# Performance work log

Measured on AMD Instinct MI355X. Metric: run time of the kernel, lower is better.

## Reference

```python
import jax, jax.numpy as jnp
import numpy as np

N_NODES = 100000
N_EDGES = 1600000
HID = 128


def setup_inputs() -> dict:
    key = jax.random.key(0)
    k1, k2, k3, k4, k5 = jax.random.split(key, 5)
    node_embeddings = jax.random.normal(k1, (N_NODES, HID), dtype=jnp.float32)
    src_idx = jax.random.randint(k2, (N_EDGES,), 0, N_NODES, dtype=jnp.int64)
    tgt_idx = jax.random.randint(k3, (N_EDGES,), 0, N_NODES, dtype=jnp.int64)
    # Params of the selected edge-type predictor (Linear(2h,h) -> ReLU -> Linear(h,1))
    W1 = jax.random.normal(k4, (2 * HID, HID), dtype=jnp.float32) * (1.0 / np.sqrt(2 * HID))
    b1 = jnp.zeros((HID,), dtype=jnp.float32)
    W2 = jax.random.normal(k5, (HID, 1), dtype=jnp.float32) * (1.0 / np.sqrt(HID))
    b2 = jnp.zeros((1,), dtype=jnp.float32)
    return {
        "node_embeddings": node_embeddings,
        "src_idx": src_idx,
        "tgt_idx": tgt_idx,
        "edge_type_idx": 0,
        "W1": W1,
        "b1": b1,
        "W2": W2,
        "b2": b2,
    }


def reference(node_embeddings, src_idx, tgt_idx, edge_type_idx, W1, b1, W2, b2):
    # edge_type_idx selects a predictor; params passed in are that predictor's.
    src_emb = node_embeddings[src_idx]  # [E, H]
    tgt_emb = node_embeddings[tgt_idx]  # [E, H]
    # cat([src,tgt]) @ W1 == src @ W1[:H] + tgt @ W1[H:]  (avoids materializing pair_feat)
    h = jax.nn.relu(src_emb @ W1[:HID] + tgt_emb @ W1[HID:] + b1)  # [E, H]
    out = h @ W2 + b2  # [E, 1]
    return out[:, 0]  # squeeze(-1) -> [E]
```

## Files before the change

kernel.cpp:

```cpp
#include <hip/hip_runtime.h>
#include <hip/hip_bf16.h>

#define HID 128

typedef __attribute__((ext_vector_type(8))) short short8;
typedef __attribute__((ext_vector_type(4))) float f32x4;
typedef __attribute__((ext_vector_type(16))) float f32x16;
typedef __attribute__((ext_vector_type(4))) unsigned int u32x4;
typedef __attribute__((ext_vector_type(2))) _Float16 h2;

__device__ __forceinline__ short f2bf(float x) {
    __bf16 b = (__bf16)x;
    return __builtin_bit_cast(short, b);
}


__global__ void pack_w1_uv_kernel(const float* __restrict__ W1, short* __restrict__ bpk2,
                                  int* __restrict__ zero128) {
    if (zero128 && blockIdx.x == 0 && threadIdx.x < 128) zero128[threadIdx.x] = 0;
    int t = blockIdx.x * 256 + threadIdx.x;
    int l    = t & 63;
    int ks   = (t >> 6) & 7;
    int nt   = (t >> 9) & 3;
    int half = t >> 11;
    int k0  = half * 128 + ks * 16 + (l >> 5) * 8;
    int col = nt * 32 + (l & 31);
    short8 v;
#pragma unroll
    for (int j = 0; j < 8; ++j)
        v[j] = f2bf(W1[(k0 + j) * HID + col]);
    *reinterpret_cast<short8*>(&bpk2[t * 8]) = v;
}

__global__ __launch_bounds__(512, 4) void uv_kernel(
    const float* __restrict__ emb,
    const short* __restrict__ bpk2,
    unsigned short* __restrict__ U,
    unsigned short* __restrict__ V,
    int Nn)
{
    __shared__ short lds_b[32768];

    const int tid = threadIdx.x;
    const int l   = tid & 63;
    const int wid = tid >> 6;
    const int wg  = wid >> 1;
    const int wn  = wid & 1;
    const int lc  = l & 31;
    const int hi  = l >> 5;

    {
        const u32x4* g = (const u32x4*)bpk2;
        u32x4* d = (u32x4*)lds_b;
#pragma unroll
        for (int i = 0; i < 8; ++i) d[i * 512 + tid] = g[i * 512 + tid];
    }
    __syncthreads();

    const int base = blockIdx.x * 128 + wg * 32;
    int nr = base + lc;
    if (nr >= Nn) nr = Nn - 1;

    f32x16 accU[2], accV[2];
#pragma unroll
    for (int n = 0; n < 2; ++n) { accU[n] = (f32x16)(0.f); accV[n] = (f32x16)(0.f); }

#pragma unroll
    for (int ks = 0; ks < 8; ++ks) {
        const float* p = emb + (size_t)nr * HID + ks * 16 + hi * 8;
        f32x4 x0 = *reinterpret_cast<const f32x4*>(p);
        f32x4 x1 = *reinterpret_cast<const f32x4*>(p + 4);
        short8 afr;
#pragma unroll
        for (int j = 0; j < 4; ++j) { afr[j] = f2bf(x0[j]); afr[4 + j] = f2bf(x1[j]); }
#pragma unroll
        for (int n = 0; n < 2; ++n) {
            const int nt = wn * 2 + n;
            short8 bU = *reinterpret_cast<const short8*>(&lds_b[(((0 + nt) * 8 + ks) * 64 + l) * 8]);
            short8 bV = *reinterpret_cast<const short8*>(&lds_b[(((4 + nt) * 8 + ks) * 64 + l) * 8]);
            accU[n] = __builtin_amdgcn_mfma_f32_32x32x16_bf16(afr, bU, accU[n], 0, 0, 0);
            accV[n] = __builtin_amdgcn_mfma_f32_32x32x16_bf16(afr, bV, accV[n], 0, 0, 0);
        }
    }

#pragma unroll
    for (int n = 0; n < 2; ++n) {
        const int col = wn * 64 + n * 32 + lc;
#pragma unroll
        for (int r = 0; r < 16; ++r) {
            const int row = (r & 3) + 8 * (r >> 2) + 4 * hi;
            const int node = base + row;
            if (node < Nn) {
                _Float16 hu = (_Float16)accU[n][r];
                _Float16 hv = (_Float16)accV[n][r];
                U[(size_t)node * HID + col] = __builtin_bit_cast(unsigned short, hu);
                V[(size_t)node * HID + col] = __builtin_bit_cast(unsigned short, hv);
            }
        }
    }
}

__global__ __launch_bounds__(256) void hist64_kernel(
    const void* __restrict__ src_raw, const void* __restrict__ tgt_raw,
    int E, float bscale, int* __restrict__ gh)
{
    __shared__ int lh[64];
    const int tid = threadIdx.x;
    if (tid < 64) lh[tid] = 0;
    __syncthreads();

    int i64f = 1;
    {
        const int* s32 = (const int*)src_raw;
#pragma unroll
        for (int i = 1; i < 32; i += 2) i64f &= (s32[i] == 0);
    }
    const int stride = gridDim.x * 256;
    for (int e = blockIdx.x * 256 + tid; e < E; e += stride) {
        int t = i64f ? (int)((const long long*)tgt_raw)[e]
                     : ((const int*)tgt_raw)[e];
        int b = (int)((float)t * bscale);
        b = b < 0 ? 0 : (b > 63 ? 63 : b);
        atomicAdd(&lh[b], 1);
    }
    __syncthreads();
    if (tid < 64 && lh[tid]) atomicAdd(&gh[tid], lh[tid]);
}

__global__ __launch_bounds__(256) void scatter64_kernel(
    const void* __restrict__ src_raw, const void* __restrict__ tgt_raw,
    int E, float bscale,
    const int* __restrict__ gh, int* __restrict__ cursor,
    int2* __restrict__ st, int* __restrict__ ei)
{
    __shared__ int lh[64], lh2[64], lo[64], grb[64], go[64];
    __shared__ int2 sST[2048];
    __shared__ int sE[2048];
    __shared__ unsigned char bkk[2048];

    const int tid = threadIdx.x;
    int i64f = 1;
    {
        const int* s32 = (const int*)src_raw;
#pragma unroll
        for (int i = 1; i < 32; i += 2) i64f &= (s32[i] == 0);
    }
    if (tid < 64) { lh[tid] = 0; lh2[tid] = 0; }
    __syncthreads();

    const int base = blockIdx.x * 2048;
    int myS[8], myT[8], myB[8];
#pragma unroll
    for (int k = 0; k < 8; ++k) {
        const int e = base + k * 256 + tid;
        myB[k] = -1;
        if (e < E) {
            int s, t;
            if (i64f) {
                s = (int)((const long long*)src_raw)[e];
                t = (int)((const long long*)tgt_raw)[e];
            } else {
                s = ((const int*)src_raw)[e];
                t = ((const int*)tgt_raw)[e];
            }
            int b = (int)((float)t * bscale);
            b = b < 0 ? 0 : (b > 63 ? 63 : b);
            myS[k] = s; myT[k] = t; myB[k] = b;
            atomicAdd(&lh[b], 1);
        }
    }
    __syncthreads();
    if (tid < 64) {
        int vl = lh[tid], vg = gh[tid];
        int il = vl, ig = vg;
#pragma unroll
        for (int off = 1; off < 64; off <<= 1) {
            int xl = __shfl_up(il, off, 64);
            int xg = __shfl_up(ig, off, 64);
            if (tid >= off) { il += xl; ig += xg; }
        }
        lo[tid] = il - vl;
        go[tid] = ig - vg;
        grb[tid] = (vl > 0) ? atomicAdd(&cursor[tid], vl) : 0;
    }
    __syncthreads();
#pragma unroll
    for (int k = 0; k < 8; ++k) {
        if (myB[k] >= 0) {
            const int b = myB[k];
            const int pl = lo[b] + atomicAdd(&lh2[b], 1);
            sST[pl] = make_int2(myS[k], myT[k]);
            sE[pl] = base + k * 256 + tid;
            bkk[pl] = (unsigned char)b;
        }
    }
    __syncthreads();
    const int total = lo[63] + lh[63];
    for (int i = tid; i < total; i += 256) {
        const int b = bkk[i];
        const int dst = go[b] + grb[b] + (i - lo[b]);
        st[dst] = sST[i];
        ei[dst] = sE[i];
    }
}

__global__ __launch_bounds__(256) void edge_pass_part_kernel(
    const unsigned short* __restrict__ U,
    const unsigned short* __restrict__ V,
    const int2* __restrict__ st,
    const int* __restrict__ ei,
    const int* __restrict__ gh,
    const float* __restrict__ b1,
    const float* __restrict__ W2,
    const float* __restrict__ b2,
    float* __restrict__ out,
    int per_x)
{
    __shared__ int sh_off8[9];

    const int tid = threadIdx.x;
    if (tid < 64) {
        int v = gh[tid];
        int inc = v;
#pragma unroll
        for (int off = 1; off < 64; off <<= 1) {
            int x = __shfl_up(inc, off, 64);
            if (tid >= off) inc += x;
        }
        if ((tid & 7) == 0) sh_off8[tid >> 3] = inc - v;
        if (tid == 63) sh_off8[8] = inc;
    }
    __syncthreads();

    const int l   = tid & 63;
    const int wid = tid >> 6;
    const int le  = l >> 4;
    const int lc  = l & 15;
    const int p   = blockIdx.x & 7;
    const int r   = blockIdx.x >> 3;

    const int pbeg = sh_off8[p];
    const int pend = sh_off8[p + 1];

    h2 b1p[4], w2p[4];
    {
        f32x4 a = *reinterpret_cast<const f32x4*>(b1 + lc * 8);
        f32x4 b = *reinterpret_cast<const f32x4*>(b1 + lc * 8 + 4);
        f32x4 c = *reinterpret_cast<const f32x4*>(W2 + lc * 8);
        f32x4 d = *reinterpret_cast<const f32x4*>(W2 + lc * 8 + 4);
#pragma unroll
        for (int j = 0; j < 2; ++j) {
            b1p[0][j] = (_Float16)a[j];     b1p[1][j] = (_Float16)a[2 + j];
            b1p[2][j] = (_Float16)b[j];     b1p[3][j] = (_Float16)b[2 + j];
            w2p[0][j] = (_Float16)c[j];     w2p[1][j] = (_Float16)c[2 + j];
            w2p[2][j] = (_Float16)d[j];     w2p[3][j] = (_Float16)d[2 + j];
        }
    }
    const float b2s = b2[0];
    const h2 zero2 = (h2)((_Float16)0.f);

    for (int base = pbeg + r * 64; base < pend; base += per_x * 64) {
        short8 ub[4], vb[4];
        int oid[4];
        bool live[4];
#pragma unroll
        for (int g = 0; g < 4; ++g) {
            int pos = base + wid * 16 + g * 4 + le;
            live[g] = (pos < pend);
            if (!live[g]) pos = base;
            const int2 pr = st[pos];
            oid[g] = ei[pos];
            ub[g] = *reinterpret_cast<const short8*>(U + (unsigned)pr.x * HID + lc * 8);
            vb[g] = *reinterpret_cast<const short8*>(V + (unsigned)pr.y * HID + lc * 8);
        }

#pragma unroll
        for (int g = 0; g < 4; ++g) {
            const unsigned int* uw = (const unsigned int*)&ub[g];
            const unsigned int* vw = (const unsigned int*)&vb[g];
            h2 s2 = zero2;
#pragma unroll
            for (int j = 0; j < 4; ++j) {
                h2 hu = __builtin_bit_cast(h2, uw[j]);
                h2 hv = __builtin_bit_cast(h2, vw[j]);
                h2 h  = hu + hv + b1p[j];
                h = __builtin_elementwise_max(h, zero2);
                s2 = s2 + h * w2p[j];
            }
            float s = (float)s2[0] + (float)s2[1];
#pragma unroll
            for (int w = 1; w < 16; w <<= 1)
                s += __shfl_xor(s, w, 16);
            if (lc == 0 && live[g])
                out[oid[g]] = s + b2s;
        }
    }
}

__global__ __launch_bounds__(256) void edge_pass_kernel(
    const unsigned short* __restrict__ U,
    const unsigned short* __restrict__ V,
    const void* __restrict__ src_raw,
    const void* __restrict__ tgt_raw,
    const float* __restrict__ b1,
    const float* __restrict__ W2,
    const float* __restrict__ b2,
    float* __restrict__ out,
    int E)
{
    const int tid = threadIdx.x;
    const int l   = tid & 63;
    const int wid = tid >> 6;
    const int le  = l >> 4;
    const int lc  = l & 15;

    int oddw = 0;
    {
        const int* s32 = (const int*)src_raw;
        if (l < 32) oddw = s32[2 * l + 1];
    }
    const bool i64f = (__ballot(oddw != 0) == 0ULL);

    h2 b1p[4], w2p[4];
    {
        f32x4 a = *reinterpret_cast<const f32x4*>(b1 + lc * 8);
        f32x4 b = *reinterpret_cast<const f32x4*>(b1 + lc * 8 + 4);
        f32x4 c = *reinterpret_cast<const f32x4*>(W2 + lc * 8);
        f32x4 d = *reinterpret_cast<const f32x4*>(W2 + lc * 8 + 4);
#pragma unroll
        for (int j = 0; j < 2; ++j) {
            b1p[0][j] = (_Float16)a[j];     b1p[1][j] = (_Float16)a[2 + j];
            b1p[2][j] = (_Float16)b[j];     b1p[3][j] = (_Float16)b[2 + j];
            w2p[0][j] = (_Float16)c[j];     w2p[1][j] = (_Float16)c[2 + j];
            w2p[2][j] = (_Float16)d[j];     w2p[3][j] = (_Float16)d[2 + j];
        }
    }
    const float b2s = b2[0];
    const h2 zero2 = (h2)((_Float16)0.f);

    const long long ebase = ((long long)blockIdx.x * 4 + wid) * 16;

    short8 ub[4], vb[4];
#pragma unroll
    for (int g = 0; g < 4; ++g) {
        long long e = ebase + g * 4 + le;
        if (e >= E) e = E - 1;
        long long si, ti;
        if (i64f) {
            si = ((const long long*)src_raw)[e];
            ti = ((const long long*)tgt_raw)[e];
        } else {
            si = ((const int*)src_raw)[e];
            ti = ((const int*)tgt_raw)[e];
        }
        ub[g] = *reinterpret_cast<const short8*>(U + (unsigned)si * HID + lc * 8);
        vb[g] = *reinterpret_cast<const short8*>(V + (unsigned)ti * HID + lc * 8);
    }

#pragma unroll
    for (int g = 0; g < 4; ++g) {
        const unsigned int* uw = (const unsigned int*)&ub[g];
        const unsigned int* vw = (const unsigned int*)&vb[g];
        h2 s2 = zero2;
#pragma unroll
        for (int j = 0; j < 4; ++j) {
            h2 hu = __builtin_bit_cast(h2, uw[j]);
            h2 hv = __builtin_bit_cast(h2, vw[j]);
            h2 h  = hu + hv + b1p[j];
            h = __builtin_elementwise_max(h, zero2);
            s2 = s2 + h * w2p[j];
        }
        float s = (float)s2[0] + (float)s2[1];
#pragma unroll
        for (int w = 1; w < 16; w <<= 1)
            s += __shfl_xor(s, w, 16);
        const long long e = ebase + g * 4 + le;
        if (lc == 0 && e < E)
            out[e] = s + b2s;
    }
}


__global__ void pack_w1_kernel(const float* __restrict__ W1, short* __restrict__ bpk) {
    int t = blockIdx.x * 256 + threadIdx.x;
    int f = (t >> 6) & 7;
    int l = t & 63;
    int n = t >> 9;
    int c = l & 15, kb = l >> 4;
    int k0 = f * 32 + kb * 8;
    short8 v;
#pragma unroll
    for (int j = 0; j < 8; ++j)
        v[j] = f2bf(W1[(k0 + j) * HID + n * 16 + c]);
    *reinterpret_cast<short8*>(&bpk[t * 8]) = v;
}

__global__ __launch_bounds__(256) void conv_emb_kernel(
    const float* __restrict__ emb, short* __restrict__ bemb, int n8) {
    int i = blockIdx.x * 256 + threadIdx.x;
    if (i >= n8) return;
    f32x4 x0 = *reinterpret_cast<const f32x4*>(emb + (size_t)i * 8);
    f32x4 x1 = *reinterpret_cast<const f32x4*>(emb + (size_t)i * 8 + 4);
    short8 v;
#pragma unroll
    for (int j = 0; j < 4; ++j) {
        v[j]     = f2bf(x0[j]);
        v[4 + j] = f2bf(x1[j]);
    }
    *reinterpret_cast<short8*>(&bemb[(size_t)i * 8]) = v;
}

template <int MODE>
__global__ __launch_bounds__(512, 4) void edge_head_kernel(
    const float* __restrict__ emb,
    const short* __restrict__ bemb,
    const void* __restrict__ src_raw,
    const void* __restrict__ tgt_raw,
    const float* __restrict__ W1,
    const float* __restrict__ b1,
    const float* __restrict__ W2,
    const float* __restrict__ b2,
    const short* __restrict__ bpk,
    float* __restrict__ out,
    int E)
{
    __shared__ short lds_b[32768];

    const int tid = threadIdx.x;

    int i64f = 1;
    {
        const int* s32 = (const int*)src_raw;
#pragma unroll
        for (int i = 1; i < 32; i += 2) i64f &= (s32[i] == 0);
    }

    if (MODE != 2) {
        const u32x4* g = (const u32x4*)bpk;
        u32x4* d = (u32x4*)lds_b;
#pragma unroll
        for (int i = 0; i < 8; ++i) d[i * 512 + tid] = g[i * 512 + tid];
    } else {
        for (int i = 0; i < 64; ++i) {
            int idx = i * 512 + tid;
            int col = idx & 127;
            int k   = idx >> 7;
            int n = col >> 4, cc = col & 15;
            int f = k >> 5, kb = (k >> 3) & 3, j = k & 7;
            int l2 = kb * 16 + cc;
            lds_b[(((n * 8 + f) * 64 + l2) << 3) + j] = f2bf(W1[idx]);
        }
    }
    __syncthreads();

    const int l = tid & 63;
    const int wid = tid >> 6;
    const int c = l & 15;
    const int g = l >> 4;
    const long long e0 = (long long)blockIdx.x * 256 + wid * 32;

    unsigned so[2], to[2];
#pragma unroll
    for (int m = 0; m < 2; ++m) {
        long long e = e0 + m * 16 + c;
        if (e >= E) e = E - 1;
        long long si, ti;
        if (i64f) {
            si = ((const long long*)src_raw)[e];
            ti = ((const long long*)tgt_raw)[e];
        } else {
            si = ((const int*)src_raw)[e];
            ti = ((const int*)tgt_raw)[e];
        }
        so[m] = (unsigned)si * HID;
        to[m] = (unsigned)ti * HID;
    }

    f32x4 acc[2][8];
#pragma unroll
    for (int m = 0; m < 2; ++m)
#pragma unroll
        for (int n = 0; n < 8; ++n)
            acc[m][n] = (f32x4){0.f, 0.f, 0.f, 0.f};

    const int koff = g * 8;
#pragma unroll
    for (int f = 0; f < 8; ++f) {
        short8 afr[2];
        const int k0 = (f & 3) * 32 + koff;
#pragma unroll
        for (int m = 0; m < 2; ++m) {
            const unsigned off = (f < 4 ? so[m] : to[m]) + k0;
            if (MODE == 0) {
                afr[m] = *reinterpret_cast<const short8*>(bemb + off);
            } else {
                f32x4 x0 = *reinterpret_cast<const f32x4*>(emb + off);
                f32x4 x1 = *reinterpret_cast<const f32x4*>(emb + off + 4);
                short8 t;
#pragma unroll
                for (int j = 0; j < 4; ++j) {
                    t[j]     = f2bf(x0[j]);
                    t[4 + j] = f2bf(x1[j]);
                }
                afr[m] = t;
            }
        }
#pragma unroll
        for (int n = 0; n < 8; ++n) {
            short8 bfr = *reinterpret_cast<const short8*>(&lds_b[((n * 8 + f) * 64 + l) * 8]);
#pragma unroll
            for (int m = 0; m < 2; ++m)
                acc[m][n] = __builtin_amdgcn_mfma_f32_16x16x32_bf16(afr[m], bfr, acc[m][n], 0, 0, 0);
        }
    }

    float b1v[8], w2v[8];
#pragma unroll
    for (int n = 0; n < 8; ++n) {
        b1v[n] = b1[n * 16 + c];
        w2v[n] = W2[n * 16 + c];
    }
    const float b2s = b2[0];

#pragma unroll
    for (int m = 0; m < 2; ++m) {
        float s[4] = {0.f, 0.f, 0.f, 0.f};
#pragma unroll
        for (int n = 0; n < 8; ++n) {
#pragma unroll
            for (int r = 0; r < 4; ++r)
                s[r] += fmaxf(acc[m][n][r] + b1v[n], 0.f) * w2v[n];
        }
#pragma unroll
        for (int w = 1; w < 16; w <<= 1) {
#pragma unroll
            for (int r = 0; r < 4; ++r)
                s[r] += __shfl_xor(s[r], w, 16);
        }
        if (c == 0) {
            const long long eb = e0 + m * 16 + g * 4;
#pragma unroll
            for (int r = 0; r < 4; ++r)
                if (eb + r < E) out[eb + r] = s[r] + b2s;
        }
    }
}

extern "C" void kernel_launch(void* const* d_in, const int* in_sizes, int n_in,
                              void* d_out, int out_size, void* d_ws, size_t ws_size,
                              hipStream_t stream) {
    const float* emb = (const float*)d_in[0];
    const void*  src = d_in[1];
    const void*  tgt = d_in[2];
    const float* W1 = (const float*)d_in[4];
    const float* b1 = (const float*)d_in[5];
    const float* W2 = (const float*)d_in[6];
    const float* b2 = (const float*)d_in[7];
    float* out = (float*)d_out;

    const int E  = in_sizes[1];
    const int Nn = in_sizes[0] / HID;

    const size_t uv_bytes = (size_t)Nn * HID * sizeof(short);
    const size_t off_gh   = 65536;
    const size_t off_U    = 65536 + 4096;
    const size_t off_V    = off_U + uv_bytes;
    const size_t off_st   = off_V + uv_bytes;
    const size_t off_ei   = off_st + (size_t)E * 8;
    const size_t need_part = off_ei + (size_t)E * 4;
    const size_t need_uv   = 65536 + 2 * uv_bytes;
    const size_t need_old  = 65536 + (size_t)in_sizes[0] * sizeof(short);

    if (ws_size >= need_part && E >= 4096) {
        short*          bpk2   = (short*)d_ws;
        int*            gh     = (int*)((char*)d_ws + off_gh);
        int*            cursor = gh + 64;
        unsigned short* U      = (unsigned short*)((char*)d_ws + off_U);
        unsigned short* Vv     = (unsigned short*)((char*)d_ws + off_V);
        int2*           st     = (int2*)((char*)d_ws + off_st);
        int*            ei     = (int*)((char*)d_ws + off_ei);

        const float bscale = 63.9999f / (float)Nn;

        pack_w1_uv_kernel<<<16, 256, 0, stream>>>(W1, bpk2, gh);
        hist64_kernel<<<256, 256, 0, stream>>>(src, tgt, E, bscale, gh);
        uv_kernel<<<(Nn + 127) / 128, 512, 0, stream>>>(emb, bpk2, U, Vv, Nn);
        scatter64_kernel<<<(E + 2047) / 2048, 256, 0, stream>>>(
            src, tgt, E, bscale, gh, cursor, st, ei);
        const int per_x = (E / 8 + 4096) / 64 + 2;
        edge_pass_part_kernel<<<per_x * 8, 256, 0, stream>>>(
            U, Vv, st, ei, gh, b1, W2, b2, out, per_x);
        return;
    }

    if (ws_size >= need_uv) {
        short*          bpk2 = (short*)d_ws;
        unsigned short* U    = (unsigned short*)((char*)d_ws + 65536);
        unsigned short* Vv   = (unsigned short*)((char*)d_ws + 65536 + uv_bytes);

        pack_w1_uv_kernel<<<16, 256, 0, stream>>>(W1, bpk2, nullptr);
        uv_kernel<<<(Nn + 127) / 128, 512, 0, stream>>>(emb, bpk2, U, Vv, Nn);
        edge_pass_kernel<<<(E + 63) / 64, 256, 0, stream>>>(U, Vv, src, tgt, b1, W2, b2, out, E);
        return;
    }

    short* bpk  = (short*)d_ws;
    short* bemb = (short*)((char*)d_ws + 65536);

    int mode;
    if (ws_size >= need_old)        mode = 0;
    else if (ws_size >= 65536)      mode = 1;
    else                            mode = 2;

    if (mode != 2)
        pack_w1_kernel<<<16, 256, 0, stream>>>(W1, bpk);
    if (mode == 0) {
        const int n8 = in_sizes[0] / 8;
        conv_emb_kernel<<<(n8 + 255) / 256, 256, 0, stream>>>(emb, bemb, n8);
    }

    const int grid = (E + 255) / 256;
    if (mode == 0)
        edge_head_kernel<0><<<grid, 512, 0, stream>>>(emb, bemb, src, tgt, W1, b1, W2, b2, bpk, out, E);
    else if (mode == 1)
        edge_head_kernel<1><<<grid, 512, 0, stream>>>(emb, bemb, src, tgt, W1, b1, W2, b2, bpk, out, E);
    else
        edge_head_kernel<2><<<grid, 512, 0, stream>>>(emb, bemb, src, tgt, W1, b1, W2, b2, bpk, out, E);
}
```

Before: 147.5 us.

## Pack edge records into 64-bit words and fuse W1 packing with histogram

Each sorted edge record now holds the edge id, source and target node in one 64-bit word, so one array replaces the separate int2 pair and edge-id arrays. This cuts scatter writes and edge-pass index reads from 12 to 8 bytes per edge and shrinks the scatter kernel's shared memory. The W1 packing kernel is merged into the histogram kernel, and zeroing of the histogram moves to a memset, removing one launch. The packed path only works while node count fits in 17 bits and edge count in 21 bits, so it is guarded by a check.

```diff
diff --git a/kernel.cpp b/kernel.cpp
--- a/kernel.cpp
+++ b/kernel.cpp
@@ -15,21 +15,48 @@
 }
 
 
-__global__ void pack_w1_uv_kernel(const float* __restrict__ W1, short* __restrict__ bpk2,
-                                  int* __restrict__ zero128) {
-    if (zero128 && blockIdx.x == 0 && threadIdx.x < 128) zero128[threadIdx.x] = 0;
-    int t = blockIdx.x * 256 + threadIdx.x;
-    int l    = t & 63;
-    int ks   = (t >> 6) & 7;
-    int nt   = (t >> 9) & 3;
-    int half = t >> 11;
-    int k0  = half * 128 + ks * 16 + (l >> 5) * 8;
-    int col = nt * 32 + (l & 31);
-    short8 v;
-#pragma unroll
-    for (int j = 0; j < 8; ++j)
-        v[j] = f2bf(W1[(k0 + j) * HID + col]);
-    *reinterpret_cast<short8*>(&bpk2[t * 8]) = v;
+__global__ __launch_bounds__(256) void hist_pack_kernel(
+    const float* __restrict__ W1, short* __restrict__ bpk2,
+    const void* __restrict__ src_raw, const void* __restrict__ tgt_raw,
+    int E, float bscale, int* __restrict__ gh)
+{
+    const int tid = threadIdx.x;
+
+    if (blockIdx.x < 16) {
+        int t = blockIdx.x * 256 + tid;
+        int l    = t & 63;
+        int ks   = (t >> 6) & 7;
+        int nt   = (t >> 9) & 3;
+        int half = t >> 11;
+        int k0  = half * 128 + ks * 16 + (l >> 5) * 8;
+        int col = nt * 32 + (l & 31);
+        short8 v;
+#pragma unroll
+        for (int j = 0; j < 8; ++j)
+            v[j] = f2bf(W1[(k0 + j) * HID + col]);
+        *reinterpret_cast<short8*>(&bpk2[t * 8]) = v;
+    }
+
+    __shared__ int lh[64];
+    if (tid < 64) lh[tid] = 0;
+    __syncthreads();
+
+    int i64f = 1;
+    {
+        const int* s32 = (const int*)src_raw;
+#pragma unroll
+        for (int i = 1; i < 32; i += 2) i64f &= (s32[i] == 0);
+    }
+    const int stride = gridDim.x * 256;
+    for (int e = blockIdx.x * 256 + tid; e < E; e += stride) {
+        int t = i64f ? (int)((const long long*)tgt_raw)[e]
+                     : ((const int*)tgt_raw)[e];
+        int b = (int)((float)t * bscale);
+        b = b < 0 ? 0 : (b > 63 ? 63 : b);
+        atomicAdd(&lh[b], 1);
+    }
+    __syncthreads();
+    if (tid < 64 && lh[tid]) atomicAdd(&gh[tid], lh[tid]);
 }
 
 __global__ __launch_bounds__(512, 4) void uv_kernel(
@@ -100,43 +127,14 @@
     }
 }
 
-__global__ __launch_bounds__(256) void hist64_kernel(
-    const void* __restrict__ src_raw, const void* __restrict__ tgt_raw,
-    int E, float bscale, int* __restrict__ gh)
-{
-    __shared__ int lh[64];
-    const int tid = threadIdx.x;
-    if (tid < 64) lh[tid] = 0;
-    __syncthreads();
-
-    int i64f = 1;
-    {
-        const int* s32 = (const int*)src_raw;
-#pragma unroll
-        for (int i = 1; i < 32; i += 2) i64f &= (s32[i] == 0);
-    }
-    const int stride = gridDim.x * 256;
-    for (int e = blockIdx.x * 256 + tid; e < E; e += stride) {
-        int t = i64f ? (int)((const long long*)tgt_raw)[e]
-                     : ((const int*)tgt_raw)[e];
-        int b = (int)((float)t * bscale);
-        b = b < 0 ? 0 : (b > 63 ? 63 : b);
-        atomicAdd(&lh[b], 1);
-    }
-    __syncthreads();
-    if (tid < 64 && lh[tid]) atomicAdd(&gh[tid], lh[tid]);
-}
-
 __global__ __launch_bounds__(256) void scatter64_kernel(
     const void* __restrict__ src_raw, const void* __restrict__ tgt_raw,
     int E, float bscale,
     const int* __restrict__ gh, int* __restrict__ cursor,
-    int2* __restrict__ st, int* __restrict__ ei)
+    unsigned long long* __restrict__ rec)
 {
     __shared__ int lh[64], lh2[64], lo[64], grb[64], go[64];
-    __shared__ int2 sST[2048];
-    __shared__ int sE[2048];
-    __shared__ unsigned char bkk[2048];
+    __shared__ unsigned long long sR[2048];
 
     const int tid = threadIdx.x;
     int i64f = 1;
@@ -189,26 +187,26 @@
         if (myB[k] >= 0) {
             const int b = myB[k];
             const int pl = lo[b] + atomicAdd(&lh2[b], 1);
-            sST[pl] = make_int2(myS[k], myT[k]);
-            sE[pl] = base + k * 256 + tid;
-            bkk[pl] = (unsigned char)b;
+            sR[pl] = (unsigned long long)(unsigned)(base + k * 256 + tid)
+                   | ((unsigned long long)(unsigned)myS[k] << 21)
+                   | ((unsigned long long)(unsigned)myT[k] << 38);
         }
     }
     __syncthreads();
     const int total = lo[63] + lh[63];
     for (int i = tid; i < total; i += 256) {
-        const int b = bkk[i];
-        const int dst = go[b] + grb[b] + (i - lo[b]);
-        st[dst] = sST[i];
-        ei[dst] = sE[i];
+        const unsigned long long r = sR[i];
+        const int t = (int)(r >> 38);
+        int b = (int)((float)t * bscale);
+        b = b < 0 ? 0 : (b > 63 ? 63 : b);
+        rec[go[b] + grb[b] + (i - lo[b])] = r;
     }
 }
 
 __global__ __launch_bounds__(256) void edge_pass_part_kernel(
     const unsigned short* __restrict__ U,
     const unsigned short* __restrict__ V,
-    const int2* __restrict__ st,
-    const int* __restrict__ ei,
+    const unsigned long long* __restrict__ rec,
     const int* __restrict__ gh,
     const float* __restrict__ b1,
     const float* __restrict__ W2,
@@ -268,10 +266,12 @@
             int pos = base + wid * 16 + g * 4 + le;
             live[g] = (pos < pend);
             if (!live[g]) pos = base;
-            const int2 pr = st[pos];
-            oid[g] = ei[pos];
-            ub[g] = *reinterpret_cast<const short8*>(U + (unsigned)pr.x * HID + lc * 8);
-            vb[g] = *reinterpret_cast<const short8*>(V + (unsigned)pr.y * HID + lc * 8);
+            const unsigned long long rc = rec[pos];
+            oid[g] = (int)(rc & 0x1FFFFF);
+            const unsigned s = (unsigned)((rc >> 21) & 0x1FFFF);
+            const unsigned t = (unsigned)(rc >> 38);
+            ub[g] = *reinterpret_cast<const short8*>(U + s * HID + lc * 8);
+            vb[g] = *reinterpret_cast<const short8*>(V + t * HID + lc * 8);
         }
 
 #pragma unroll
@@ -565,31 +565,31 @@
     const size_t off_gh   = 65536;
     const size_t off_U    = 65536 + 4096;
     const size_t off_V    = off_U + uv_bytes;
-    const size_t off_st   = off_V + uv_bytes;
-    const size_t off_ei   = off_st + (size_t)E * 8;
-    const size_t need_part = off_ei + (size_t)E * 4;
+    const size_t off_rec  = off_V + uv_bytes;
+    const size_t need_part = off_rec + (size_t)E * 8;
     const size_t need_uv   = 65536 + 2 * uv_bytes;
     const size_t need_old  = 65536 + (size_t)in_sizes[0] * sizeof(short);
 
-    if (ws_size >= need_part && E >= 4096) {
-        short*          bpk2   = (short*)d_ws;
-        int*            gh     = (int*)((char*)d_ws + off_gh);
-        int*            cursor = gh + 64;
-        unsigned short* U      = (unsigned short*)((char*)d_ws + off_U);
-        unsigned short* Vv     = (unsigned short*)((char*)d_ws + off_V);
-        int2*           st     = (int2*)((char*)d_ws + off_st);
-        int*            ei     = (int*)((char*)d_ws + off_ei);
+    const bool packable = (Nn <= (1 << 17)) && (E <= (1 << 21));
+
+    if (ws_size >= need_part && E >= 4096 && packable) {
+        short*              bpk2   = (short*)d_ws;
+        int*                gh     = (int*)((char*)d_ws + off_gh);
+        int*                cursor = gh + 64;
+        unsigned short*     U      = (unsigned short*)((char*)d_ws + off_U);
+        unsigned short*     Vv     = (unsigned short*)((char*)d_ws + off_V);
+        unsigned long long* rec    = (unsigned long long*)((char*)d_ws + off_rec);
 
         const float bscale = 63.9999f / (float)Nn;
 
-        pack_w1_uv_kernel<<<16, 256, 0, stream>>>(W1, bpk2, gh);
-        hist64_kernel<<<256, 256, 0, stream>>>(src, tgt, E, bscale, gh);
+        hipMemsetAsync(gh, 0, 512, stream);
+        hist_pack_kernel<<<256, 256, 0, stream>>>(W1, bpk2, src, tgt, E, bscale, gh);
         uv_kernel<<<(Nn + 127) / 128, 512, 0, stream>>>(emb, bpk2, U, Vv, Nn);
         scatter64_kernel<<<(E + 2047) / 2048, 256, 0, stream>>>(
-            src, tgt, E, bscale, gh, cursor, st, ei);
+            src, tgt, E, bscale, gh, cursor, rec);
         const int per_x = (E / 8 + 4096) / 64 + 2;
         edge_pass_part_kernel<<<per_x * 8, 256, 0, stream>>>(
-            U, Vv, st, ei, gh, b1, W2, b2, out, per_x);
+            U, Vv, rec, gh, b1, W2, b2, out, per_x);
         return;
     }
 
@@ -598,7 +598,7 @@
         unsigned short* U    = (unsigned short*)((char*)d_ws + 65536);
         unsigned short* Vv   = (unsigned short*)((char*)d_ws + 65536 + uv_bytes);
 
-        pack_w1_uv_kernel<<<16, 256, 0, stream>>>(W1, bpk2, nullptr);
+        hist_pack_kernel<<<16, 256, 0, stream>>>(W1, bpk2, src, tgt, 0, 1.0f, nullptr);
         uv_kernel<<<(Nn + 127) / 128, 512, 0, stream>>>(emb, bpk2, U, Vv, Nn);
         edge_pass_kernel<<<(E + 63) / 64, 256, 0, stream>>>(U, Vv, src, tgt, b1, W2, b2, out, E);
         return;
```

After: 145.2 us. About the same (-1.5%).
